# Performance work log

Measured on AMD Instinct MI355X. Metric: run time of the kernel, lower is better.

Reference implementation:

```python
import jax, jax.numpy as jnp
import numpy as np

IN_F, OUT_F = 256, 256
GRID, ORDER = 5, 3
K = GRID + ORDER + 1  # 9 knots
EPS_MINMAX = 1e-7     # K.epsilon()
EPS_BN = 1e-3         # keras BatchNormalization default epsilon


def setup_inputs() -> dict:
    key = jax.random.key(0)
    ks = jax.random.split(key, 4)
    x = jax.random.normal(ks[0], (32, 32, 32, IN_F), dtype=jnp.float32)
    he = lambda k, shape, fan_in: jax.random.normal(k, shape, jnp.float32) * np.sqrt(2.0 / fan_in)
    base_weight = he(ks[1], (IN_F, OUT_F), IN_F)
    spline_weight = he(ks[2], (OUT_F, IN_F, K), IN_F * K)
    spline_scaler = jnp.ones((OUT_F, IN_F), jnp.float32)
    return {
        'x': x,
        'base_weight': base_weight,
        'spline_weight': spline_weight,
        'spline_scaler': spline_scaler,
        'bn_base_gamma': jnp.ones((OUT_F,), jnp.float32),
        'bn_base_beta': jnp.zeros((OUT_F,), jnp.float32),
        'bn_base_mean': jnp.zeros((OUT_F,), jnp.float32),
        'bn_base_var': jnp.ones((OUT_F,), jnp.float32),
        'bn_spline_gamma': jnp.ones((OUT_F,), jnp.float32),
        'bn_spline_beta': jnp.zeros((OUT_F,), jnp.float32),
        'bn_spline_mean': jnp.zeros((OUT_F,), jnp.float32),
        'bn_spline_var': jnp.ones((OUT_F,), jnp.float32),
    }


def _bn(z, gamma, beta, mean, var):
    # Keras BatchNormalization, inference mode (training=False)
    return gamma * (z - mean) * jax.lax.rsqrt(var + EPS_BN) + beta


def reference(x, base_weight, spline_weight, spline_scaler,
              bn_base_gamma, bn_base_beta, bn_base_mean, bn_base_var,
              bn_spline_gamma, bn_spline_beta, bn_spline_mean, bn_spline_var):
    B, H, W, _ = x.shape
    xf = x.reshape(-1, IN_F)  # [N, in]

    # base path: GEMM -> BN -> SiLU
    base = xf @ base_weight
    base = jax.nn.silu(_bn(base, bn_base_gamma, bn_base_beta, bn_base_mean, bn_base_var))

    # min-max normalize per feature over the flattened batch
    x_min = jnp.min(xf, axis=0, keepdims=True)
    x_max = jnp.max(xf, axis=0, keepdims=True)
    xn = (xf - x_min) / (x_max - x_min + EPS_MINMAX)

    # triangle basis: relu(1 - |x - knot|), knots = linspace(-1, 1, K)
    knots = jnp.linspace(-1.0, 1.0, K, dtype=jnp.float32)
    basis = jnp.maximum(0.0, 1.0 - jnp.abs(xn[:, :, None] - knots[None, None, :]))  # [N, in, K]

    # scaled spline weight, flattened GEMM
    w = (spline_weight * spline_scaler[:, :, None]).reshape(OUT_F, IN_F * K)  # [out, in*K]
    spline = basis.reshape(-1, IN_F * K) @ w.T  # [N, out]
    spline = _bn(spline, bn_spline_gamma, bn_spline_beta, bn_spline_mean, bn_spline_var)

    out = base + spline
    return out.reshape(B, H, W, OUT_F)
```

## Files before the change

### kernel.cpp

```cpp
#include <hip/hip_runtime.h>
#include <stdint.h>
#include <stddef.h>

typedef _Float16 h2 __attribute__((ext_vector_type(2)));
typedef _Float16 h8 __attribute__((ext_vector_type(8)));
typedef float f4 __attribute__((ext_vector_type(4)));

union Hfrag { h2 p[4]; h8 v; };

#define WS_PMIN   0
#define WS_PMAX   524288
#define WS_BT     0
#define WS_SMALL  1310720
#define WS_MINV   (WS_SMALL + 0)
#define WS_SCALEV (WS_SMALL + 1024)
#define WS_BSC    (WS_SMALL + 2048)
#define WS_BSH    (WS_SMALL + 3072)
#define WS_SSC    (WS_SMALL + 4096)
#define WS_SSH    (WS_SMALL + 5120)

__global__ __launch_bounds__(256) void kan_minmax(const float* __restrict__ x,
                                                  float* __restrict__ pmin,
                                                  float* __restrict__ pmax) {
  __shared__ f4 smn[4][64], smx[4][64];
  const int b = blockIdx.x, t = threadIdx.x;
  const int fq = t & 63, rg = t >> 6;
  const float* p = x + (size_t)b * 64 * 256 + (size_t)rg * 16 * 256 + fq * 4;
  f4 mn = (f4)(3.402823466e38f), mx = (f4)(-3.402823466e38f);
#pragma unroll
  for (int j = 0; j < 16; ++j) {
    f4 v = *(const f4*)(p + (size_t)j * 256);
    mn = __builtin_elementwise_min(mn, v);
    mx = __builtin_elementwise_max(mx, v);
  }
  smn[rg][fq] = mn; smx[rg][fq] = mx;
  __syncthreads();
  if (rg == 0) {
#pragma unroll
    for (int g = 1; g < 4; ++g) {
      mn = __builtin_elementwise_min(mn, smn[g][fq]);
      mx = __builtin_elementwise_max(mx, smx[g][fq]);
    }
    *(f4*)(pmin + (size_t)b * 256 + fq * 4) = mn;
    *(f4*)(pmax + (size_t)b * 256 + fq * 4) = mx;
  }
}

__global__ __launch_bounds__(256) void kan_finalize(
    const float* __restrict__ pmin, const float* __restrict__ pmax,
    const float* __restrict__ g1, const float* __restrict__ b1,
    const float* __restrict__ m1, const float* __restrict__ v1,
    const float* __restrict__ g2, const float* __restrict__ b2,
    const float* __restrict__ m2, const float* __restrict__ v2,
    float* __restrict__ minv, float* __restrict__ scalev,
    float* __restrict__ bscv, float* __restrict__ bshv,
    float* __restrict__ sscv, float* __restrict__ sshv) {
  __shared__ float smn[4][64], smx[4][64];
  const int t = threadIdx.x;
  const int ol = t & 63, pg = t >> 6;
  const int o = blockIdx.x * 64 + ol;
  float mn = 3.402823466e38f, mx = -3.402823466e38f;
  for (int p = pg * 128; p < pg * 128 + 128; ++p) {
    mn = fminf(mn, pmin[(size_t)p * 256 + o]);
    mx = fmaxf(mx, pmax[(size_t)p * 256 + o]);
  }
  smn[pg][ol] = mn; smx[pg][ol] = mx;
  __syncthreads();
  if (pg == 0) {
#pragma unroll
    for (int g = 1; g < 4; ++g) {
      mn = fminf(mn, smn[g][ol]);
      mx = fmaxf(mx, smx[g][ol]);
    }
    minv[o] = mn;
    scalev[o] = 1.0f / (mx - mn + 1e-7f);
    const float bs = g1[o] / sqrtf(v1[o] + 1e-3f);
    bscv[o] = bs;
    bshv[o] = b1[o] - m1[o] * bs;
    const float ss = g2[o] / sqrtf(v2[o] + 1e-3f);
    sscv[o] = ss;
    sshv[o] = b2[o] - m2[o] * ss;
  }
}

__global__ __launch_bounds__(256) void kan_buildw(
    const float* __restrict__ spline_w, const float* __restrict__ spline_s,
    const float* __restrict__ base_w, _Float16* __restrict__ Bt) {
  const int gid = blockIdx.x * 256 + threadIdx.x;
  const int f = gid * 4;
  const int ks = f >> 13;
  const int rem = f & 8191;
  const int half = rem >> 12;
  const int rem2 = rem & 4095;
  const int o = rem2 >> 5;
  const int kk = rem2 & 31;
  const int og = half * 128 + o;
  float v[4];
  if (ks < 72) {
    const int k = ks >> 3;
    const int i0 = ((ks & 7) << 5) + kk;
#pragma unroll
    for (int j = 0; j < 4; ++j) {
      const int i = i0 + j;
      v[j] = spline_w[(size_t)(og * 256 + i) * 9 + k] * spline_s[og * 256 + i];
    }
  } else {
    const int i0 = (ks - 72) * 32 + kk;
#pragma unroll
    for (int j = 0; j < 4; ++j) {
      const int i = i0 + j;
      v[j] = base_w[(size_t)i * 256 + og];
    }
  }
  union { _Float16 h[4]; uint2 u; } pk;
#pragma unroll
  for (int j = 0; j < 4; ++j) pk.h[j] = (_Float16)v[j];
  *(uint2*)(Bt + f) = pk.u;
}

__global__ __launch_bounds__(256, 2) void kan_gemm(
    const float* __restrict__ x, const _Float16* __restrict__ Bt,
    const float* __restrict__ minv, const float* __restrict__ scalev,
    const float* __restrict__ bscv, const float* __restrict__ bshv,
    const float* __restrict__ sscv, const float* __restrict__ sshv,
    float* __restrict__ out) {
  const int tid = threadIdx.x;
  const int lane = tid & 63;
  const int wv = tid >> 6;
  const int wm = wv >> 1, wn = wv & 1;
  const int lr = lane & 15, lg = lane >> 4;
  const int mt = blockIdx.x & 255, nt = blockIdx.x >> 8;

  const int rowA = mt * 128 + wm * 64 + lr;
  const int colB = wn * 64 + lr;

  f4 accS[4][4], accB[4][4];
#pragma unroll
  for (int m = 0; m < 4; ++m)
#pragma unroll
    for (int n = 0; n < 4; ++n) { accS[m][n] = (f4)0.0f; accB[m][n] = (f4)0.0f; }

  const char* btbase = (const char*)Bt + (size_t)nt * 8192 + (size_t)colB * 64 + (size_t)lg * 16;

  f4 xa[4], xb[4], mn0, mn1, sc0, sc1;

  {
    const int ib = lg * 8;
#pragma unroll
    for (int m = 0; m < 4; ++m) {
      const float* px = x + (size_t)(rowA + m * 16) * 256 + ib;
      xa[m] = *(const f4*)px; xb[m] = *(const f4*)(px + 4);
    }
    mn0 = *(const f4*)(minv + ib);  mn1 = *(const f4*)(minv + ib + 4);
    sc0 = *(const f4*)(scalev + ib); sc1 = *(const f4*)(scalev + ib + 4);
  }

#pragma unroll 1
  for (int ic = 0; ic < 8; ++ic) {
    Hfrag xn[4];
#pragma unroll
    for (int m = 0; m < 4; ++m) {
      f4 na = (xa[m] - mn0) * sc0;
      f4 nb = (xb[m] - mn1) * sc1;
      xn[m].p[0][0] = (_Float16)na.x; xn[m].p[0][1] = (_Float16)na.y;
      xn[m].p[1][0] = (_Float16)na.z; xn[m].p[1][1] = (_Float16)na.w;
      xn[m].p[2][0] = (_Float16)nb.x; xn[m].p[2][1] = (_Float16)nb.y;
      xn[m].p[3][0] = (_Float16)nb.z; xn[m].p[3][1] = (_Float16)nb.w;
    }
#pragma unroll
    for (int it = 0; it < 9; ++it) {
      const int cks = (it < 8) ? ((it + 1) * 8 + ic) : (72 + ic);
      const char* bp = btbase + (size_t)cks * 16384;
      Hfrag bf[4];
#pragma unroll
      for (int n = 0; n < 4; ++n)
        bf[n].v = *(const h8*)(bp + n * 1024);
      if (it < 8) {
        const float t = -1.0f + 0.25f * (float)(it + 1);
        const _Float16 c1 = (_Float16)(1.0f + t);
        const _Float16 c2 = (_Float16)(1.0f - t);
        h2 hc1; hc1[0] = c1; hc1[1] = c1;
        h2 hc2; hc2[0] = c2; hc2[1] = c2;
        h2 hz;  hz[0] = (_Float16)0.0f; hz[1] = (_Float16)0.0f;
        Hfrag af[4];
#pragma unroll
        for (int m = 0; m < 4; ++m) {
#pragma unroll
          for (int q = 0; q < 4; ++q) {
            h2 xv = xn[m].p[q];
            h2 u = hc1 - xv;
            h2 w = hc2 + xv;
            af[m].p[q] = __builtin_elementwise_max(__builtin_elementwise_min(u, w), hz);
          }
        }
#pragma unroll
        for (int m = 0; m < 4; ++m)
#pragma unroll
          for (int n = 0; n < 4; ++n)
            accS[m][n] = __builtin_amdgcn_mfma_f32_16x16x32_f16(af[m].v, bf[n].v, accS[m][n], 0, 0, 0);
      } else {
        Hfrag af[4];
#pragma unroll
        for (int m = 0; m < 4; ++m) {
          af[m].p[0][0] = (_Float16)xa[m].x; af[m].p[0][1] = (_Float16)xa[m].y;
          af[m].p[1][0] = (_Float16)xa[m].z; af[m].p[1][1] = (_Float16)xa[m].w;
          af[m].p[2][0] = (_Float16)xb[m].x; af[m].p[2][1] = (_Float16)xb[m].y;
          af[m].p[3][0] = (_Float16)xb[m].z; af[m].p[3][1] = (_Float16)xb[m].w;
        }
#pragma unroll
        for (int m = 0; m < 4; ++m)
#pragma unroll
          for (int n = 0; n < 4; ++n)
            accB[m][n] = __builtin_amdgcn_mfma_f32_16x16x32_f16(af[m].v, bf[n].v, accB[m][n], 0, 0, 0);
        if (ic < 7) {
          const int ib = (ic + 1) * 32 + lg * 8;
#pragma unroll
          for (int m = 0; m < 4; ++m) {
            const float* px = x + (size_t)(rowA + m * 16) * 256 + ib;
            xa[m] = *(const f4*)px; xb[m] = *(const f4*)(px + 4);
          }
          mn0 = *(const f4*)(minv + ib);  mn1 = *(const f4*)(minv + ib + 4);
          sc0 = *(const f4*)(scalev + ib); sc1 = *(const f4*)(scalev + ib + 4);
        }
      }
    }
  }

#pragma unroll
  for (int n = 0; n < 4; ++n) {
    const int col = nt * 128 + colB + n * 16;
    const float vbs = bscv[col], vbh = bshv[col];
    const float vss = sscv[col], vsh = sshv[col];
#pragma unroll
    for (int m = 0; m < 4; ++m) {
      const int row0 = mt * 128 + wm * 64 + m * 16 + lg * 4;
#pragma unroll
      for (int r = 0; r < 4; ++r) {
        const float zb = accB[m][n][r] * vbs + vbh;
        const float si = zb / (1.0f + __expf(-zb));
        const float val = si + accS[m][n][r] * vss + vsh;
        out[(size_t)(row0 + r) * 256 + col] = val;
      }
    }
  }
}

extern "C" void kernel_launch(void* const* d_in, const int* in_sizes, int n_in,
                              void* d_out, int out_size, void* d_ws, size_t ws_size,
                              hipStream_t stream) {
  const float* x        = (const float*)d_in[0];
  const float* base_w   = (const float*)d_in[1];
  const float* spline_w = (const float*)d_in[2];
  const float* spline_s = (const float*)d_in[3];
  const float* g1 = (const float*)d_in[4];
  const float* b1 = (const float*)d_in[5];
  const float* m1 = (const float*)d_in[6];
  const float* v1 = (const float*)d_in[7];
  const float* g2 = (const float*)d_in[8];
  const float* b2 = (const float*)d_in[9];
  const float* m2 = (const float*)d_in[10];
  const float* v2 = (const float*)d_in[11];
  float* out = (float*)d_out;
  char* ws = (char*)d_ws;

  float* pmin   = (float*)(ws + WS_PMIN);
  float* pmax   = (float*)(ws + WS_PMAX);
  _Float16* Bt  = (_Float16*)(ws + WS_BT);
  float* minv   = (float*)(ws + WS_MINV);
  float* scalev = (float*)(ws + WS_SCALEV);
  float* bscv   = (float*)(ws + WS_BSC);
  float* bshv   = (float*)(ws + WS_BSH);
  float* sscv   = (float*)(ws + WS_SSC);
  float* sshv   = (float*)(ws + WS_SSH);

  kan_minmax<<<512, 256, 0, stream>>>(x, pmin, pmax);
  kan_finalize<<<4, 256, 0, stream>>>(pmin, pmax, g1, b1, m1, v1, g2, b2, m2, v2,
                                      minv, scalev, bscv, bshv, sscv, sshv);
  kan_buildw<<<640, 256, 0, stream>>>(spline_w, spline_s, base_w, Bt);
  kan_gemm<<<512, 256, 0, stream>>>(x, Bt, minv, scalev, bscv, bshv, sscv, sshv, out);
}
```

Measured before the change: 168.0 us.

## Halve GEMM M-tile, raise occupancy, and normalize x in fp16 with reconstructed base input

The GEMM block tile shrinks from 128 to 64 rows, the grid doubles to 1024 blocks, and launch bounds go to four blocks per CU to cut register pressure and raise occupancy. Blocks are swizzled so groups of eight M-tiles share both N-tiles for locality. Min-max normalization now runs in packed fp16 with fp16 min, scale and range vectors. The base-path input is rebuilt from the normalized value as xn*range+min instead of keeping the fp32 x registers. This removes register prefetching of x and adds fp16 rounding error to both paths, especially the reconstructed base input.

```diff
diff --git a/kernel.cpp b/kernel.cpp
--- a/kernel.cpp
+++ b/kernel.cpp
@@ -12,12 +12,13 @@
 #define WS_PMAX   524288
 #define WS_BT     0
 #define WS_SMALL  1310720
-#define WS_MINV   (WS_SMALL + 0)
-#define WS_SCALEV (WS_SMALL + 1024)
-#define WS_BSC    (WS_SMALL + 2048)
-#define WS_BSH    (WS_SMALL + 3072)
-#define WS_SSC    (WS_SMALL + 4096)
-#define WS_SSH    (WS_SMALL + 5120)
+#define WS_BSC    (WS_SMALL + 0)
+#define WS_BSH    (WS_SMALL + 1024)
+#define WS_SSC    (WS_SMALL + 2048)
+#define WS_SSH    (WS_SMALL + 3072)
+#define WS_MINH   (WS_SMALL + 4096)
+#define WS_SCH    (WS_SMALL + 4608)
+#define WS_RGH    (WS_SMALL + 5120)
 
 __global__ __launch_bounds__(256) void kan_minmax(const float* __restrict__ x,
                                                   float* __restrict__ pmin,
@@ -52,9 +53,10 @@
     const float* __restrict__ m1, const float* __restrict__ v1,
     const float* __restrict__ g2, const float* __restrict__ b2,
     const float* __restrict__ m2, const float* __restrict__ v2,
-    float* __restrict__ minv, float* __restrict__ scalev,
     float* __restrict__ bscv, float* __restrict__ bshv,
-    float* __restrict__ sscv, float* __restrict__ sshv) {
+    float* __restrict__ sscv, float* __restrict__ sshv,
+    _Float16* __restrict__ minh, _Float16* __restrict__ sch,
+    _Float16* __restrict__ rgh) {
   __shared__ float smn[4][64], smx[4][64];
   const int t = threadIdx.x;
   const int ol = t & 63, pg = t >> 6;
@@ -72,8 +74,10 @@
       mn = fminf(mn, smn[g][ol]);
       mx = fmaxf(mx, smx[g][ol]);
     }
-    minv[o] = mn;
-    scalev[o] = 1.0f / (mx - mn + 1e-7f);
+    const float range = mx - mn + 1e-7f;
+    minh[o] = (_Float16)mn;
+    sch[o]  = (_Float16)(1.0f / range);
+    rgh[o]  = (_Float16)range;
     const float bs = g1[o] / sqrtf(v1[o] + 1e-3f);
     bscv[o] = bs;
     bshv[o] = b1[o] - m1[o] * bs;
@@ -118,9 +122,10 @@
   *(uint2*)(Bt + f) = pk.u;
 }
 
-__global__ __launch_bounds__(256, 2) void kan_gemm(
+__global__ __launch_bounds__(256, 4) void kan_gemm(
     const float* __restrict__ x, const _Float16* __restrict__ Bt,
-    const float* __restrict__ minv, const float* __restrict__ scalev,
+    const _Float16* __restrict__ minh, const _Float16* __restrict__ sch,
+    const _Float16* __restrict__ rgh,
     const float* __restrict__ bscv, const float* __restrict__ bshv,
     const float* __restrict__ sscv, const float* __restrict__ sshv,
     float* __restrict__ out) {
@@ -129,43 +134,42 @@
   const int wv = tid >> 6;
   const int wm = wv >> 1, wn = wv & 1;
   const int lr = lane & 15, lg = lane >> 4;
-  const int mt = blockIdx.x & 255, nt = blockIdx.x >> 8;
-
-  const int rowA = mt * 128 + wm * 64 + lr;
+  const int j = blockIdx.x & 15, g = blockIdx.x >> 4;
+  const int mt = g * 8 + (j & 7);
+  const int nt = j >> 3;
+
+  const int rowA = mt * 64 + wm * 32 + lr;
   const int colB = wn * 64 + lr;
 
-  f4 accS[4][4], accB[4][4];
-#pragma unroll
-  for (int m = 0; m < 4; ++m)
+  f4 accS[2][4], accB[2][4];
+#pragma unroll
+  for (int m = 0; m < 2; ++m)
 #pragma unroll
     for (int n = 0; n < 4; ++n) { accS[m][n] = (f4)0.0f; accB[m][n] = (f4)0.0f; }
 
   const char* btbase = (const char*)Bt + (size_t)nt * 8192 + (size_t)colB * 64 + (size_t)lg * 16;
-
-  f4 xa[4], xb[4], mn0, mn1, sc0, sc1;
-
-  {
-    const int ib = lg * 8;
-#pragma unroll
-    for (int m = 0; m < 4; ++m) {
-      const float* px = x + (size_t)(rowA + m * 16) * 256 + ib;
-      xa[m] = *(const f4*)px; xb[m] = *(const f4*)(px + 4);
-    }
-    mn0 = *(const f4*)(minv + ib);  mn1 = *(const f4*)(minv + ib + 4);
-    sc0 = *(const f4*)(scalev + ib); sc1 = *(const f4*)(scalev + ib + 4);
-  }
 
 #pragma unroll 1
   for (int ic = 0; ic < 8; ++ic) {
-    Hfrag xn[4];
-#pragma unroll
-    for (int m = 0; m < 4; ++m) {
-      f4 na = (xa[m] - mn0) * sc0;
-      f4 nb = (xb[m] - mn1) * sc1;
-      xn[m].p[0][0] = (_Float16)na.x; xn[m].p[0][1] = (_Float16)na.y;
-      xn[m].p[1][0] = (_Float16)na.z; xn[m].p[1][1] = (_Float16)na.w;
-      xn[m].p[2][0] = (_Float16)nb.x; xn[m].p[2][1] = (_Float16)nb.y;
-      xn[m].p[3][0] = (_Float16)nb.z; xn[m].p[3][1] = (_Float16)nb.w;
+    const int ib = ic * 32 + lg * 8;
+    Hfrag mh, sh, rh;
+    mh.v = *(const h8*)(minh + ib);
+    sh.v = *(const h8*)(sch + ib);
+    rh.v = *(const h8*)(rgh + ib);
+    Hfrag xn[2];
+#pragma unroll
+    for (int m = 0; m < 2; ++m) {
+      const float* px = x + (size_t)(rowA + m * 16) * 256 + ib;
+      f4 a = *(const f4*)px;
+      f4 b = *(const f4*)(px + 4);
+      h2 h0; h0[0] = (_Float16)a.x; h0[1] = (_Float16)a.y;
+      h2 h1; h1[0] = (_Float16)a.z; h1[1] = (_Float16)a.w;
+      h2 h2v; h2v[0] = (_Float16)b.x; h2v[1] = (_Float16)b.y;
+      h2 h3; h3[0] = (_Float16)b.z; h3[1] = (_Float16)b.w;
+      xn[m].p[0] = (h0 - mh.p[0]) * sh.p[0];
+      xn[m].p[1] = (h1 - mh.p[1]) * sh.p[1];
+      xn[m].p[2] = (h2v - mh.p[2]) * sh.p[2];
+      xn[m].p[3] = (h3 - mh.p[3]) * sh.p[3];
     }
 #pragma unroll
     for (int it = 0; it < 9; ++it) {
@@ -175,6 +179,7 @@
 #pragma unroll
       for (int n = 0; n < 4; ++n)
         bf[n].v = *(const h8*)(bp + n * 1024);
+      Hfrag af[2];
       if (it < 8) {
         const float t = -1.0f + 0.25f * (float)(it + 1);
         const _Float16 c1 = (_Float16)(1.0f + t);
@@ -182,9 +187,8 @@
         h2 hc1; hc1[0] = c1; hc1[1] = c1;
         h2 hc2; hc2[0] = c2; hc2[1] = c2;
         h2 hz;  hz[0] = (_Float16)0.0f; hz[1] = (_Float16)0.0f;
-        Hfrag af[4];
-#pragma unroll
-        for (int m = 0; m < 4; ++m) {
+#pragma unroll
+        for (int m = 0; m < 2; ++m) {
 #pragma unroll
           for (int q = 0; q < 4; ++q) {
             h2 xv = xn[m].p[q];
@@ -194,46 +198,34 @@
           }
         }
 #pragma unroll
-        for (int m = 0; m < 4; ++m)
+        for (int m = 0; m < 2; ++m)
 #pragma unroll
           for (int n = 0; n < 4; ++n)
             accS[m][n] = __builtin_amdgcn_mfma_f32_16x16x32_f16(af[m].v, bf[n].v, accS[m][n], 0, 0, 0);
       } else {
-        Hfrag af[4];
-#pragma unroll
-        for (int m = 0; m < 4; ++m) {
-          af[m].p[0][0] = (_Float16)xa[m].x; af[m].p[0][1] = (_Float16)xa[m].y;
-          af[m].p[1][0] = (_Float16)xa[m].z; af[m].p[1][1] = (_Float16)xa[m].w;
-          af[m].p[2][0] = (_Float16)xb[m].x; af[m].p[2][1] = (_Float16)xb[m].y;
-          af[m].p[3][0] = (_Float16)xb[m].z; af[m].p[3][1] = (_Float16)xb[m].w;
+#pragma unroll
+        for (int m = 0; m < 2; ++m) {
+#pragma unroll
+          for (int q = 0; q < 4; ++q)
+            af[m].p[q] = xn[m].p[q] * rh.p[q] + mh.p[q];
         }
 #pragma unroll
-        for (int m = 0; m < 4; ++m)
+        for (int m = 0; m < 2; ++m)
 #pragma unroll
           for (int n = 0; n < 4; ++n)
             accB[m][n] = __builtin_amdgcn_mfma_f32_16x16x32_f16(af[m].v, bf[n].v, accB[m][n], 0, 0, 0);
-        if (ic < 7) {
-          const int ib = (ic + 1) * 32 + lg * 8;
-#pragma unroll
-          for (int m = 0; m < 4; ++m) {
-            const float* px = x + (size_t)(rowA + m * 16) * 256 + ib;
-            xa[m] = *(const f4*)px; xb[m] = *(const f4*)(px + 4);
-          }
-          mn0 = *(const f4*)(minv + ib);  mn1 = *(const f4*)(minv + ib + 4);
-          sc0 = *(const f4*)(scalev + ib); sc1 = *(const f4*)(scalev + ib + 4);
-        }
       }
     }
   }
 
 #pragma unroll
   for (int n = 0; n < 4; ++n) {
-    const int col = nt * 128 + colB + n * 16;
+    const int col = nt * 128 + wn * 64 + n * 16 + lr;
     const float vbs = bscv[col], vbh = bshv[col];
     const float vss = sscv[col], vsh = sshv[col];
 #pragma unroll
-    for (int m = 0; m < 4; ++m) {
-      const int row0 = mt * 128 + wm * 64 + m * 16 + lg * 4;
+    for (int m = 0; m < 2; ++m) {
+      const int row0 = mt * 64 + wm * 32 + m * 16 + lg * 4;
 #pragma unroll
       for (int r = 0; r < 4; ++r) {
         const float zb = accB[m][n][r] * vbs + vbh;
@@ -266,16 +258,18 @@
   float* pmin   = (float*)(ws + WS_PMIN);
   float* pmax   = (float*)(ws + WS_PMAX);
   _Float16* Bt  = (_Float16*)(ws + WS_BT);
-  float* minv   = (float*)(ws + WS_MINV);
-  float* scalev = (float*)(ws + WS_SCALEV);
   float* bscv   = (float*)(ws + WS_BSC);
   float* bshv   = (float*)(ws + WS_BSH);
   float* sscv   = (float*)(ws + WS_SSC);
   float* sshv   = (float*)(ws + WS_SSH);
+  _Float16* minh = (_Float16*)(ws + WS_MINH);
+  _Float16* sch  = (_Float16*)(ws + WS_SCH);
+  _Float16* rgh  = (_Float16*)(ws + WS_RGH);
 
   kan_minmax<<<512, 256, 0, stream>>>(x, pmin, pmax);
   kan_finalize<<<4, 256, 0, stream>>>(pmin, pmax, g1, b1, m1, v1, g2, b2, m2, v2,
-                                      minv, scalev, bscv, bshv, sscv, sshv);
+                                      bscv, bshv, sscv, sshv, minh, sch, rgh);
   kan_buildw<<<640, 256, 0, stream>>>(spline_w, spline_s, base_w, Bt);
-  kan_gemm<<<512, 256, 0, stream>>>(x, Bt, minv, scalev, bscv, bshv, sscv, sshv, out);
-}
+  kan_gemm<<<1024, 256, 0, stream>>>(x, Bt, minh, sch, rgh,
+                                     bscv, bshv, sscv, sshv, out);
+}
```

After: 197.4 us. +17.5%, slower.
